# Kernel optimization log

Measured on AMD Instinct MI355X. Metric: run time of the kernel, lower is better.

## Reference

```python
import jax, jax.numpy as jnp
import numpy as np

THR = 0.001
EPS = 1e-5
GROUPS = 32

def ternary_weight(w):
    wc = jnp.clip(w, -1.0, 1.0)
    return jnp.where(wc > THR, 1.0, jnp.where(wc < -THR, -1.0, 0.0))

def fake_quant(x, scale):
    s = jnp.abs(scale)
    return jnp.clip(jnp.round(x / s), -1.0, 1.0) * s

def group_norm(x, gamma, beta):
    b, c, h, w = x.shape
    xg = x.reshape(b, GROUPS, c // GROUPS, h, w)
    mu = xg.mean(axis=(2, 3, 4), keepdims=True)
    var = xg.var(axis=(2, 3, 4), keepdims=True)
    xn = (xg - mu) * jax.lax.rsqrt(var + EPS)
    return xn.reshape(b, c, h, w) * gamma[None, :, None, None] + beta[None, :, None, None]

def conv2d(x, w, b, pad):
    out = jax.lax.conv_general_dilated(x, w, (1, 1), [(pad, pad), (pad, pad)],
                                       dimension_numbers=('NCHW', 'OIHW', 'NCHW'))
    return out + b[None, :, None, None]

def setup_inputs() -> dict:
    key = jax.random.key(0)
    ks = jax.random.split(key, 10)
    B, Cin, Cout, H, W, T = 8, 256, 256, 64, 64, 512
    return {
        'x': jax.random.normal(ks[0], (B, Cin, H, W), jnp.float32),
        'time_emb': jax.random.normal(ks[1], (B, T), jnp.float32),
        'gn1_g': jnp.ones((Cin,), jnp.float32),
        'gn1_b': jnp.zeros((Cin,), jnp.float32),
        'scale1': jnp.array(1.0, jnp.float32),
        'W1': jax.random.normal(ks[2], (Cout, Cin, 3, 3), jnp.float32) * 0.05,
        'b1': jax.random.normal(ks[3], (Cout,), jnp.float32) * 0.01,
        'Wt': jax.random.normal(ks[4], (Cout, T), jnp.float32) * 0.05,
        'bt': jax.random.normal(ks[5], (Cout,), jnp.float32) * 0.01,
        'gn2_g': jnp.ones((Cout,), jnp.float32),
        'gn2_b': jnp.zeros((Cout,), jnp.float32),
        'scale2': jnp.array(1.0, jnp.float32),
        'W2': jax.random.normal(ks[6], (Cout, Cout, 3, 3), jnp.float32) * 0.05,
        'b2': jax.random.normal(ks[7], (Cout,), jnp.float32) * 0.01,
    }

def reference(x, time_emb, gn1_g, gn1_b, scale1, W1, b1, Wt, bt, gn2_g, gn2_b, scale2, W2, b2):
    out = group_norm(x, gn1_g, gn1_b)
    out = jax.nn.relu(out)
    out = fake_quant(out, scale1)
    out = conv2d(out, ternary_weight(W1), b1, pad=1)
    # time conditioning: ternary linear on relu(time_emb), broadcast over HW
    tb = jax.nn.relu(time_emb) @ ternary_weight(Wt).T + bt
    out = out + tb[:, :, None, None]
    out = group_norm(out, gn2_g, gn2_b)
    out = jax.nn.relu(out)
    out = fake_quant(out, scale2)
    out = conv2d(out, ternary_weight(W2), b2, pad=1)
    # dropout p=0 (eval) and identity residual (in_channels == out_channels)
    return out + x
```

## Files before the change

### kernel.cpp

```cpp
#include <hip/hip_runtime.h>

typedef float f32x4 __attribute__((ext_vector_type(4)));
typedef __bf16 bf16x8 __attribute__((ext_vector_type(8)));
typedef unsigned int u32;

#define WTHR 0.001f

static constexpr size_t WS_A1   = 0;
static constexpr size_t WS_A2   = 16777216;
static constexpr size_t WS_OUT1 = 33554432;
static constexpr size_t WS_TW   = 67108864;
static constexpr size_t WS_TB   = 69468160;
static constexpr size_t WS_GN1  = 69476352;
static constexpr size_t WS_GN2  = 69478400;

__global__ __launch_bounds__(256)
void k_gn_stats(const float* __restrict__ x, float* __restrict__ mean, float* __restrict__ rstd)
{
    int bg = blockIdx.x;
    int t = threadIdx.x;
    int lane = t & 63, wv = t >> 6;
    const float4* A = reinterpret_cast<const float4*>(x + (size_t)bg * 32768 + (size_t)t * 128);
    __shared__ float red[4];
    __shared__ float Mv;

    float r0, r1, r2, r3, r4, r5, r6, r7;
    {
        float4 v0 = A[0], v1 = A[1];
        r0 = v0.x; r1 = v0.y; r2 = v0.z; r3 = v0.w;
        r4 = v1.x; r5 = v1.y; r6 = v1.z; r7 = v1.w;
        for (int i = 2; i < 32; i += 2) {
            float4 u0 = A[i], u1 = A[i + 1];
            r0 += u0.x; r1 += u0.y; r2 += u0.z; r3 += u0.w;
            r4 += u1.x; r5 += u1.y; r6 += u1.z; r7 += u1.w;
        }
    }
    float p = ((r0 + r1) + (r2 + r3)) + ((r4 + r5) + (r6 + r7));
    #pragma unroll
    for (int st = 1; st <= 32; st <<= 1) p = p + __shfl_down(p, st);
    if (lane == 0) red[wv] = p;
    __syncthreads();
    if (t == 0) Mv = ((red[0] + red[1]) + (red[2] + red[3])) / 32768.0f;
    __syncthreads();
    float mn = Mv;

    {
        float4 v0 = A[0], v1 = A[1];
        float d;
        d = v0.x - mn; r0 = __fmul_rn(d, d);
        d = v0.y - mn; r1 = __fmul_rn(d, d);
        d = v0.z - mn; r2 = __fmul_rn(d, d);
        d = v0.w - mn; r3 = __fmul_rn(d, d);
        d = v1.x - mn; r4 = __fmul_rn(d, d);
        d = v1.y - mn; r5 = __fmul_rn(d, d);
        d = v1.z - mn; r6 = __fmul_rn(d, d);
        d = v1.w - mn; r7 = __fmul_rn(d, d);
        for (int i = 2; i < 32; i += 2) {
            float4 u0 = A[i], u1 = A[i + 1];
            d = u0.x - mn; r0 = r0 + __fmul_rn(d, d);
            d = u0.y - mn; r1 = r1 + __fmul_rn(d, d);
            d = u0.z - mn; r2 = r2 + __fmul_rn(d, d);
            d = u0.w - mn; r3 = r3 + __fmul_rn(d, d);
            d = u1.x - mn; r4 = r4 + __fmul_rn(d, d);
            d = u1.y - mn; r5 = r5 + __fmul_rn(d, d);
            d = u1.z - mn; r6 = r6 + __fmul_rn(d, d);
            d = u1.w - mn; r7 = r7 + __fmul_rn(d, d);
        }
    }
    p = ((r0 + r1) + (r2 + r3)) + ((r4 + r5) + (r6 + r7));
    #pragma unroll
    for (int st = 1; st <= 32; st <<= 1) p = p + __shfl_down(p, st);
    if (lane == 0) red[wv] = p;
    __syncthreads();
    if (t == 0) {
        float var = ((red[0] + red[1]) + (red[2] + red[3])) / 32768.0f;
        mean[bg] = mn;
        rstd[bg] = __fdiv_rn(1.0f, __fsqrt_rn(var + 1e-5f));
    }
}

__global__ __launch_bounds__(256)
void k_tern(const float* __restrict__ W1, const float* __restrict__ W2, unsigned short* __restrict__ twT)
{
    int blk = blockIdx.x;
    int co = blk & 255;
    const float* src = ((blk & 256) ? W2 : W1) + (size_t)co * 2304;
    unsigned short* base = twT + (size_t)(blk >> 8) * 589824 + (co << 8);
    int t = threadIdx.x;
    __shared__ unsigned short Q[2304];
    #pragma unroll
    for (int i = 0; i < 9; ++i) {
        float w = src[t + (i << 8)];
        Q[t + (i << 8)] = (w > WTHR) ? (unsigned short)0x3F80u
                        : ((w < -WTHR) ? (unsigned short)0xBF80u : (unsigned short)0u);
    }
    __syncthreads();
    #pragma unroll
    for (int i = 0; i < 9; ++i) {
        int idx = t + (i << 8);
        int off = idx >> 8, ci = idx & 255;
        base[off * 65536 + ci] = Q[ci * 9 + off];
    }
}

__global__ __launch_bounds__(256)
void k_tb(const float* __restrict__ te, const float* __restrict__ Wt, const float* __restrict__ bt,
          float* __restrict__ tb)
{
    int b = blockIdx.x, co = threadIdx.x;
    const float* wrow = Wt + (size_t)co * 512;
    const float* trow = te + (size_t)b * 512;
    float acc = 0.f;
    for (int t = 0; t < 512; ++t) {
        float w = wrow[t];
        float tw = (w > WTHR) ? 1.f : ((w < -WTHR) ? -1.f : 0.f);
        acc = __fmaf_rn(fmaxf(trow[t], 0.f), tw, acc);
    }
    tb[(b << 8) + co] = acc + bt[co];
}

__global__ __launch_bounds__(256)
void k_norm_quant(const float* __restrict__ x, const float* __restrict__ gamma, const float* __restrict__ beta,
                  const float* __restrict__ mean, const float* __restrict__ rstd,
                  const float* __restrict__ scale, unsigned short* __restrict__ a)
{
    int blk = blockIdx.x;
    int b = blk >> 6, h = blk & 63;
    int tid = threadIdx.x;
    __shared__ unsigned short T[64 * 256];
    float s = fabsf(*scale);
    int w = tid & 63;
    int g0 = (tid >> 6) << 3;
    #pragma unroll
    for (int o = 0; o < 8; ++o) {
        int gc = g0 + o;
        alignas(16) unsigned short r8[8];
        float mnv = mean[(b << 5) + gc], rsv = rstd[(b << 5) + gc];
        #pragma unroll
        for (int j = 0; j < 8; ++j) {
            int c = (gc << 3) + j;
            float xv = x[((size_t)((b << 8) + c) << 12) + (h << 6) + w];
            float y = __fmul_rn(xv - mnv, rsv);
            y = y * gamma[c] + beta[c];
            y = fmaxf(y, 0.f);
            r8[j] = (rintf(__fdiv_rn(y, s)) >= 1.0f) ? (unsigned short)0x3F80u : (unsigned short)0u;
        }
        int gs = gc ^ (w & 31);
        *reinterpret_cast<uint4*>(&T[(w << 8) + (gs << 3)]) = *reinterpret_cast<const uint4*>(r8);
    }
    __syncthreads();
    unsigned short* dst = a + ((size_t)blk << 14);
    #pragma unroll
    for (int j = 0; j < 8; ++j) {
        int e = (j << 11) + (tid << 3);
        int ww = e >> 8;
        int gs = (tid & 31) ^ (ww & 31);
        *reinterpret_cast<uint4*>(dst + e) = *reinterpret_cast<const uint4*>(&T[(ww << 8) + (gs << 3)]);
    }
}

template<int O>
__global__ __launch_bounds__(256, 4)
void k_conv(const unsigned short* __restrict__ acts,
            const unsigned short* __restrict__ twT,
            const float* __restrict__ bias,
            const float* __restrict__ tb,
            const float* __restrict__ scale,
            const float* __restrict__ resid,
            float* __restrict__ out)
{
    int blk0 = blockIdx.x;
    int logical = ((blk0 & 7) << 7) + (blk0 >> 3);
    int half = logical & 1;
    int bh = logical >> 1;
    int b = bh >> 6, h = bh & 63;
    int tid = threadIdx.x;
    int lane = tid & 63, wv = tid >> 6;
    int l15 = lane & 15, l4 = lane >> 4;

    __shared__ unsigned short Ls[3 * 64 * 64];

    f32x4 acc[2][4];
    #pragma unroll
    for (int i = 0; i < 2; ++i)
        #pragma unroll
        for (int j = 0; j < 4; ++j) acc[i][j] = (f32x4){0.f, 0.f, 0.f, 0.f};

    int lw = lane >> 3;
    int lc = (lane & 7) ^ lw;
    int cobase = (half << 7) + (wv << 5);

    for (int cc = 0; cc < 4; ++cc) {
        __syncthreads();
        #pragma unroll
        for (int i = 0; i < 6; ++i) {
            int chunk = wv * 6 + i;
            int dh = chunk >> 3;
            int w0 = (chunk & 7) << 3;
            int hh = h + dh - 1;
            char* ldst = (char*)Ls + chunk * 1024;
            if ((unsigned)hh < 64u) {
                const unsigned short* g = acts
                    + ((size_t)(((b << 6) + hh) << 6) + (w0 + lw)) * 256 + (cc << 6) + (lc << 3);
                __builtin_amdgcn_global_load_lds(
                    (const __attribute__((address_space(1))) u32*)g,
                    (__attribute__((address_space(3))) u32*)ldst, 16, 0, 0);
            } else {
                *reinterpret_cast<uint4*>(ldst + lane * 16) = (uint4){0u, 0u, 0u, 0u};
            }
        }
        __syncthreads();

        auto loadStep = [&](int s, bf16x8* af, bf16x8* wf) {
            int off = s >> 1;
            int kh = off / 3;
            int kwv = off % 3 - 1;
            int kk = s & 1;
            #pragma unroll
            for (int nt = 0; nt < 4; ++nt) {
                int wi = (nt << 4) + l15 + kwv;
                bool ok = (unsigned)wi < 64u;
                int wc = ok ? wi : 0;
                int byte = ((kh << 6) + wc) * 128 + (((kk << 6) + (l4 << 4)) ^ ((wc & 7) << 4));
                uint4 uv = *reinterpret_cast<const uint4*>((const char*)Ls + byte);
                u32 m = ok ? 0xFFFFFFFFu : 0u;
                uv.x &= m; uv.y &= m; uv.z &= m; uv.w &= m;
                af[nt] = *reinterpret_cast<const bf16x8*>(&uv);
            }
            const unsigned short* wb = twT + ((size_t)off << 16)
                + ((size_t)(cobase + l15) << 8) + (cc << 6) + (kk << 5) + (l4 << 3);
            wf[0] = *reinterpret_cast<const bf16x8*>(wb);
            wf[1] = *reinterpret_cast<const bf16x8*>(wb + 4096);
        };

        bf16x8 afA[4], afB[4], wfA[2], wfB[2];
        loadStep(0, afA, wfA);
        #pragma unroll
        for (int s = 0; s < 18; ++s) {
            if (s < 17) {
                if (s & 1) loadStep(s + 1, afA, wfA);
                else       loadStep(s + 1, afB, wfB);
            }
            const bf16x8* af = (s & 1) ? afB : afA;
            const bf16x8* wf = (s & 1) ? wfB : wfA;
            #pragma unroll
            for (int mt = 0; mt < 2; ++mt)
                #pragma unroll
                for (int nt = 0; nt < 4; ++nt)
                    acc[mt][nt] = __builtin_amdgcn_mfma_f32_16x16x32_bf16(wf[mt], af[nt], acc[mt][nt], 0, 0, 0);
        }
    }

    float qs = fabsf(*scale);
    #pragma unroll
    for (int mt = 0; mt < 2; ++mt)
        #pragma unroll
        for (int r = 0; r < 4; ++r) {
            int co = cobase + (mt << 4) + (l4 << 2) + r;
            float bb = bias[co];
            float tv = (O == 0) ? tb[(b << 8) + co] : 0.f;
            size_t rowb = ((size_t)((b << 8) + co) << 12) + (h << 6);
            #pragma unroll
            for (int nt = 0; nt < 4; ++nt) {
                int w = (nt << 4) + l15;
                float v = __fmul_rn(acc[mt][nt][r], qs) + bb;
                if (O == 0) v = v + tv;
                else        v = v + resid[rowb + w];
                out[rowb + w] = v;
            }
        }
}

extern "C" void kernel_launch(void* const* d_in, const int* in_sizes, int n_in,
                              void* d_out, int out_size, void* d_ws, size_t ws_size,
                              hipStream_t stream)
{
    const float* x      = (const float*)d_in[0];
    const float* te     = (const float*)d_in[1];
    const float* gn1_g  = (const float*)d_in[2];
    const float* gn1_b  = (const float*)d_in[3];
    const float* scale1 = (const float*)d_in[4];
    const float* W1     = (const float*)d_in[5];
    const float* b1     = (const float*)d_in[6];
    const float* Wt     = (const float*)d_in[7];
    const float* bt     = (const float*)d_in[8];
    const float* gn2_g  = (const float*)d_in[9];
    const float* gn2_b  = (const float*)d_in[10];
    const float* scale2 = (const float*)d_in[11];
    const float* W2     = (const float*)d_in[12];
    const float* b2     = (const float*)d_in[13];
    float* out = (float*)d_out;

    char* ws = (char*)d_ws;
    unsigned short* a1   = (unsigned short*)(ws + WS_A1);
    unsigned short* a2   = (unsigned short*)(ws + WS_A2);
    float*          out1 = (float*)(ws + WS_OUT1);
    unsigned short* tw   = (unsigned short*)(ws + WS_TW);
    unsigned short* tw1  = tw;
    unsigned short* tw2  = tw + 589824;
    float*          tbp  = (float*)(ws + WS_TB);
    float*          gn1m = (float*)(ws + WS_GN1);
    float*          gn1r = gn1m + 256;
    float*          gn2m = (float*)(ws + WS_GN2);
    float*          gn2r = gn2m + 256;

    k_gn_stats<<<256, 256, 0, stream>>>(x, gn1m, gn1r);
    k_tern<<<512, 256, 0, stream>>>(W1, W2, tw);
    k_tb<<<8, 256, 0, stream>>>(te, Wt, bt, tbp);
    k_norm_quant<<<512, 256, 0, stream>>>(x, gn1_g, gn1_b, gn1m, gn1r, scale1, a1);
    k_conv<0><<<1024, 256, 0, stream>>>(a1, tw1, b1, tbp, scale1, nullptr, out1);
    k_gn_stats<<<256, 256, 0, stream>>>(out1, gn2m, gn2r);
    k_norm_quant<<<512, 256, 0, stream>>>(out1, gn2_g, gn2_b, gn2m, gn2r, scale2, a2);
    k_conv<1><<<1024, 256, 0, stream>>>(a2, tw2, b2, nullptr, scale2, x, out);
}
```

Measured before the change: 318.7 us.

## Merge prep kernels, widen conv tile to all 256 outputs, double-buffer LDS

Three small prep kernels (GN stats, ternary weight packing, time-bias linear) become one launch. The packed weight layout changes so each 32-channel k-slice is contiguous per output channel. The conv kernel now computes all 256 output channels per block, halving the grid and reusing each staged activation row across twice as many channels. It also double-buffers the LDS activation tiles, overlapping the next channel chunk's load with the MFMA work. This raises register pressure (16 accumulators), lowers the occupancy target to 2 blocks per SIMD, and drops the previous register-level software prefetch. The LDS swizzle in norm_quant changes from XOR with 31 to XOR with 7.

After: 363.6 us. 1.14x slower.

```diff
diff --git a/kernel.cpp b/kernel.cpp
--- a/kernel.cpp
+++ b/kernel.cpp
@@ -14,15 +14,12 @@
 static constexpr size_t WS_GN1  = 69476352;
 static constexpr size_t WS_GN2  = 69478400;
 
-__global__ __launch_bounds__(256)
-void k_gn_stats(const float* __restrict__ x, float* __restrict__ mean, float* __restrict__ rstd)
-{
-    int bg = blockIdx.x;
-    int t = threadIdx.x;
+__device__ __forceinline__ void gn_stats_body(const float* __restrict__ x, float* __restrict__ mean,
+                                              float* __restrict__ rstd, int bg, int t,
+                                              float* red , float* Mv )
+{
     int lane = t & 63, wv = t >> 6;
     const float4* A = reinterpret_cast<const float4*>(x + (size_t)bg * 32768 + (size_t)t * 128);
-    __shared__ float red[4];
-    __shared__ float Mv;
 
     float r0, r1, r2, r3, r4, r5, r6, r7;
     {
@@ -40,9 +37,9 @@
     for (int st = 1; st <= 32; st <<= 1) p = p + __shfl_down(p, st);
     if (lane == 0) red[wv] = p;
     __syncthreads();
-    if (t == 0) Mv = ((red[0] + red[1]) + (red[2] + red[3])) / 32768.0f;
+    if (t == 0) *Mv = ((red[0] + red[1]) + (red[2] + red[3])) / 32768.0f;
     __syncthreads();
-    float mn = Mv;
+    float mn = *Mv;
 
     {
         float4 v0 = A[0], v1 = A[1];
@@ -80,43 +77,56 @@
 }
 
 __global__ __launch_bounds__(256)
-void k_tern(const float* __restrict__ W1, const float* __restrict__ W2, unsigned short* __restrict__ twT)
-{
+void k_gn_stats(const float* __restrict__ x, float* __restrict__ mean, float* __restrict__ rstd)
+{
+    __shared__ float red[4];
+    __shared__ float Mv;
+    gn_stats_body(x, mean, rstd, blockIdx.x, threadIdx.x, red, &Mv);
+}
+
+__global__ __launch_bounds__(256)
+void k_prep(const float* __restrict__ x, float* __restrict__ mean, float* __restrict__ rstd,
+            const float* __restrict__ W1, const float* __restrict__ W2, unsigned short* __restrict__ twT,
+            const float* __restrict__ te, const float* __restrict__ Wt, const float* __restrict__ bt,
+            float* __restrict__ tb)
+{
+    __shared__ union { struct { float red[4]; float Mv; } g; unsigned short Q[2304]; } sh;
     int blk = blockIdx.x;
-    int co = blk & 255;
-    const float* src = ((blk & 256) ? W2 : W1) + (size_t)co * 2304;
-    unsigned short* base = twT + (size_t)(blk >> 8) * 589824 + (co << 8);
     int t = threadIdx.x;
-    __shared__ unsigned short Q[2304];
-    #pragma unroll
-    for (int i = 0; i < 9; ++i) {
-        float w = src[t + (i << 8)];
-        Q[t + (i << 8)] = (w > WTHR) ? (unsigned short)0x3F80u
-                        : ((w < -WTHR) ? (unsigned short)0xBF80u : (unsigned short)0u);
-    }
-    __syncthreads();
-    #pragma unroll
-    for (int i = 0; i < 9; ++i) {
-        int idx = t + (i << 8);
-        int off = idx >> 8, ci = idx & 255;
-        base[off * 65536 + ci] = Q[ci * 9 + off];
-    }
-}
-
-__global__ __launch_bounds__(256)
-void k_tb(const float* __restrict__ te, const float* __restrict__ Wt, const float* __restrict__ bt,
-          float* __restrict__ tb)
-{
-    int b = blockIdx.x, co = threadIdx.x;
-    const float* wrow = Wt + (size_t)co * 512;
-    const float* trow = te + (size_t)b * 512;
-    float acc = 0.f;
-    for (int t = 0; t < 512; ++t) {
-        float w = wrow[t];
-        float tw = (w > WTHR) ? 1.f : ((w < -WTHR) ? -1.f : 0.f);
-        acc = __fmaf_rn(fmaxf(trow[t], 0.f), tw, acc);
-    }
-    tb[(b << 8) + co] = acc + bt[co];
+    if (blk < 256) {
+        gn_stats_body(x, mean, rstd, blk, t, sh.g.red, &sh.g.Mv);
+    } else if (blk < 768) {
+        int bb = blk - 256;
+        int co = bb & 255;
+        const float* src = ((bb & 256) ? W2 : W1) + (size_t)co * 2304;
+        unsigned short* base = twT + (size_t)(bb >> 8) * 589824;
+        #pragma unroll
+        for (int i = 0; i < 9; ++i) {
+            float w = src[t + (i << 8)];
+            sh.Q[t + (i << 8)] = (w > WTHR) ? (unsigned short)0x3F80u
+                               : ((w < -WTHR) ? (unsigned short)0xBF80u : (unsigned short)0u);
+        }
+        __syncthreads();
+        #pragma unroll
+        for (int i = 0; i < 9; ++i) {
+            int oidx = t + (i << 8);
+            int off = oidx >> 8, ci = oidx & 255;
+            size_t dst = (size_t)off * 65536 + (size_t)(ci >> 6) * 16384
+                       + (size_t)((ci >> 5) & 1) * 8192 + (size_t)co * 32 + (ci & 31);
+            base[dst] = sh.Q[ci * 9 + off];
+        }
+    } else {
+        int b = blk - 768, co = t;
+        const float* wrow = Wt + (size_t)co * 512;
+        const float* trow = te + (size_t)b * 512;
+        float acc = 0.f;
+        for (int k = 0; k < 512; ++k) {
+            float w = wrow[k];
+            float tw = (w > WTHR) ? 1.f : ((w < -WTHR) ? -1.f : 0.f);
+            acc = __fmaf_rn(fmaxf(trow[k], 0.f), tw, acc);
+        }
+        tb[(b << 8) + co] = acc + bt[co];
+    }
 }
 
 __global__ __launch_bounds__(256)
@@ -145,7 +155,7 @@
             y = fmaxf(y, 0.f);
             r8[j] = (rintf(__fdiv_rn(y, s)) >= 1.0f) ? (unsigned short)0x3F80u : (unsigned short)0u;
         }
-        int gs = gc ^ (w & 31);
+        int gs = gc ^ (w & 7);
         *reinterpret_cast<uint4*>(&T[(w << 8) + (gs << 3)]) = *reinterpret_cast<const uint4*>(r8);
     }
     __syncthreads();
@@ -154,13 +164,13 @@
     for (int j = 0; j < 8; ++j) {
         int e = (j << 11) + (tid << 3);
         int ww = e >> 8;
-        int gs = (tid & 31) ^ (ww & 31);
+        int gs = (tid & 31) ^ (ww & 7);
         *reinterpret_cast<uint4*>(dst + e) = *reinterpret_cast<const uint4*>(&T[(ww << 8) + (gs << 3)]);
     }
 }
 
 template<int O>
-__global__ __launch_bounds__(256, 4)
+__global__ __launch_bounds__(256, 2)
 void k_conv(const unsigned short* __restrict__ acts,
             const unsigned short* __restrict__ twT,
             const float* __restrict__ bias,
@@ -170,35 +180,32 @@
             float* __restrict__ out)
 {
     int blk0 = blockIdx.x;
-    int logical = ((blk0 & 7) << 7) + (blk0 >> 3);
-    int half = logical & 1;
-    int bh = logical >> 1;
-    int b = bh >> 6, h = bh & 63;
+    int logical = ((blk0 & 7) << 6) + (blk0 >> 3);
+    int b = logical >> 6, h = logical & 63;
     int tid = threadIdx.x;
     int lane = tid & 63, wv = tid >> 6;
     int l15 = lane & 15, l4 = lane >> 4;
 
-    __shared__ unsigned short Ls[3 * 64 * 64];
-
-    f32x4 acc[2][4];
-    #pragma unroll
-    for (int i = 0; i < 2; ++i)
+    __shared__ unsigned short Ls[2 * 3 * 64 * 64];
+
+    f32x4 acc[4][4];
+    #pragma unroll
+    for (int i = 0; i < 4; ++i)
         #pragma unroll
         for (int j = 0; j < 4; ++j) acc[i][j] = (f32x4){0.f, 0.f, 0.f, 0.f};
 
     int lw = lane >> 3;
     int lc = (lane & 7) ^ lw;
-    int cobase = (half << 7) + (wv << 5);
-
-    for (int cc = 0; cc < 4; ++cc) {
-        __syncthreads();
+    int cobase = wv << 6;
+
+    auto stage = [&](int cc, int buf) {
         #pragma unroll
         for (int i = 0; i < 6; ++i) {
             int chunk = wv * 6 + i;
             int dh = chunk >> 3;
             int w0 = (chunk & 7) << 3;
             int hh = h + dh - 1;
-            char* ldst = (char*)Ls + chunk * 1024;
+            char* ldst = (char*)Ls + buf * 24576 + chunk * 1024;
             if ((unsigned)hh < 64u) {
                 const unsigned short* g = acts
                     + ((size_t)(((b << 6) + hh) << 6) + (w0 + lw)) * 256 + (cc << 6) + (lc << 3);
@@ -209,51 +216,51 @@
                 *reinterpret_cast<uint4*>(ldst + lane * 16) = (uint4){0u, 0u, 0u, 0u};
             }
         }
+    };
+
+    stage(0, 0);
+    int cur = 0;
+    for (int cc = 0; cc < 4; ++cc) {
         __syncthreads();
-
-        auto loadStep = [&](int s, bf16x8* af, bf16x8* wf) {
-            int off = s >> 1;
-            int kh = off / 3;
-            int kwv = off % 3 - 1;
-            int kk = s & 1;
+        if (cc < 3) stage(cc + 1, cur ^ 1);
+        const char* Lb = (const char*)Ls + cur * 24576;
+
+        #pragma unroll
+        for (int off = 0; off < 9; ++off) {
+            const int kh = off / 3;
+            const int kw = off % 3 - 1;
             #pragma unroll
-            for (int nt = 0; nt < 4; ++nt) {
-                int wi = (nt << 4) + l15 + kwv;
-                bool ok = (unsigned)wi < 64u;
-                int wc = ok ? wi : 0;
-                int byte = ((kh << 6) + wc) * 128 + (((kk << 6) + (l4 << 4)) ^ ((wc & 7) << 4));
-                uint4 uv = *reinterpret_cast<const uint4*>((const char*)Ls + byte);
-                u32 m = ok ? 0xFFFFFFFFu : 0u;
-                uv.x &= m; uv.y &= m; uv.z &= m; uv.w &= m;
-                af[nt] = *reinterpret_cast<const bf16x8*>(&uv);
+            for (int kk = 0; kk < 2; ++kk) {
+                bf16x8 af[4], wf[4];
+                #pragma unroll
+                for (int nt = 0; nt < 4; ++nt) {
+                    int wi = (nt << 4) + l15 + kw;
+                    bool ok = (unsigned)wi < 64u;
+                    int wc = ok ? wi : 0;
+                    int byte = ((kh << 6) + wc) * 128 + (((kk << 6) + (l4 << 4)) ^ ((wc & 7) << 4));
+                    uint4 uv = *reinterpret_cast<const uint4*>(Lb + byte);
+                    u32 m = ok ? 0xFFFFFFFFu : 0u;
+                    uv.x &= m; uv.y &= m; uv.z &= m; uv.w &= m;
+                    af[nt] = *reinterpret_cast<const bf16x8*>(&uv);
+                }
+                const unsigned short* wb = twT + (size_t)off * 65536 + (size_t)cc * 16384
+                    + (size_t)kk * 8192 + (size_t)(cobase + l15) * 32 + (l4 << 3);
+                #pragma unroll
+                for (int mt = 0; mt < 4; ++mt)
+                    wf[mt] = *reinterpret_cast<const bf16x8*>(wb + mt * 512);
+                #pragma unroll
+                for (int mt = 0; mt < 4; ++mt)
+                    #pragma unroll
+                    for (int nt = 0; nt < 4; ++nt)
+                        acc[mt][nt] = __builtin_amdgcn_mfma_f32_16x16x32_bf16(wf[mt], af[nt], acc[mt][nt], 0, 0, 0);
             }
-            const unsigned short* wb = twT + ((size_t)off << 16)
-                + ((size_t)(cobase + l15) << 8) + (cc << 6) + (kk << 5) + (l4 << 3);
-            wf[0] = *reinterpret_cast<const bf16x8*>(wb);
-            wf[1] = *reinterpret_cast<const bf16x8*>(wb + 4096);
-        };
-
-        bf16x8 afA[4], afB[4], wfA[2], wfB[2];
-        loadStep(0, afA, wfA);
-        #pragma unroll
-        for (int s = 0; s < 18; ++s) {
-            if (s < 17) {
-                if (s & 1) loadStep(s + 1, afA, wfA);
-                else       loadStep(s + 1, afB, wfB);
-            }
-            const bf16x8* af = (s & 1) ? afB : afA;
-            const bf16x8* wf = (s & 1) ? wfB : wfA;
-            #pragma unroll
-            for (int mt = 0; mt < 2; ++mt)
-                #pragma unroll
-                for (int nt = 0; nt < 4; ++nt)
-                    acc[mt][nt] = __builtin_amdgcn_mfma_f32_16x16x32_bf16(wf[mt], af[nt], acc[mt][nt], 0, 0, 0);
-        }
+        }
+        cur ^= 1;
     }
 
     float qs = fabsf(*scale);
     #pragma unroll
-    for (int mt = 0; mt < 2; ++mt)
+    for (int mt = 0; mt < 4; ++mt)
         #pragma unroll
         for (int r = 0; r < 4; ++r) {
             int co = cobase + (mt << 4) + (l4 << 2) + r;
@@ -304,12 +311,10 @@
     float*          gn2m = (float*)(ws + WS_GN2);
     float*          gn2r = gn2m + 256;
 
-    k_gn_stats<<<256, 256, 0, stream>>>(x, gn1m, gn1r);
-    k_tern<<<512, 256, 0, stream>>>(W1, W2, tw);
-    k_tb<<<8, 256, 0, stream>>>(te, Wt, bt, tbp);
+    k_prep<<<776, 256, 0, stream>>>(x, gn1m, gn1r, W1, W2, tw, te, Wt, bt, tbp);
     k_norm_quant<<<512, 256, 0, stream>>>(x, gn1_g, gn1_b, gn1m, gn1r, scale1, a1);
-    k_conv<0><<<1024, 256, 0, stream>>>(a1, tw1, b1, tbp, scale1, nullptr, out1);
+    k_conv<0><<<512, 256, 0, stream>>>(a1, tw1, b1, tbp, scale1, nullptr, out1);
     k_gn_stats<<<256, 256, 0, stream>>>(out1, gn2m, gn2r);
     k_norm_quant<<<512, 256, 0, stream>>>(out1, gn2_g, gn2_b, gn2m, gn2r, scale2, a2);
-    k_conv<1><<<1024, 256, 0, stream>>>(a2, tw2, b2, nullptr, scale2, x, out);
-}
+    k_conv<1><<<512, 256, 0, stream>>>(a2, tw2, b2, nullptr, scale2, x, out);
+}
```
